# Optimization experiments

Measured on AMD Instinct MI355X. Metric: run time of the kernel, lower is better.

The kernel has to match this reference:

```python
import jax, jax.numpy as jnp
import numpy as np

N, IN_DIM, OUT_DIM = 8192, 512, 256
ALPHA = 0.2
NEG_INF = -9e15


def setup_inputs() -> dict:
    key = jax.random.key(0)
    k1, k2, k3, k4 = jax.random.split(key, 4)
    node_features = jax.random.normal(k1, (N, IN_DIM), dtype=jnp.float32)
    adj_matrix = jax.random.randint(k2, (N, N), 0, 2, dtype=jnp.int32)
    # xavier-uniform linear weight [out,in] -> store as [in,out]
    lim_w = float(np.sqrt(6.0 / (IN_DIM + OUT_DIM)))
    W = jax.random.uniform(k3, (IN_DIM, OUT_DIM), dtype=jnp.float32, minval=-lim_w, maxval=lim_w)
    b = jnp.zeros((OUT_DIM,), dtype=jnp.float32)
    # attention Linear(2*out_dim, 1): weight a [2*out_dim], bias scalar
    lim_a = float(np.sqrt(6.0 / (2 * OUT_DIM + 1)))
    a = jax.random.uniform(k4, (2 * OUT_DIM,), dtype=jnp.float32, minval=-lim_a, maxval=lim_a)
    a_bias = jnp.zeros((), dtype=jnp.float32)
    return {"adj_matrix": adj_matrix, "node_features": node_features, "W": W, "b": b, "a": a, "a_bias": a_bias}


def reference(adj_matrix, node_features, W, b, a, a_bias):
    # h = Linear(node_features); dropout is identity in eval mode
    h = node_features @ W + b                     # [N, D]
    # attention(cat(h_i, h_j)) == h_i @ a_l + h_j @ a_r + a_bias
    a_l, a_r = a[:OUT_DIM], a[OUT_DIM:]
    e_l = h @ a_l                                 # [N]
    e_r = h @ a_r                                 # [N]
    e = jax.nn.leaky_relu(e_l[:, None] + e_r[None, :] + a_bias, ALPHA)  # [N, N]
    scores = jnp.where(adj_matrix > 0, e, NEG_INF)
    attention = jax.nn.softmax(scores, axis=1)    # [N, N]
    h_prime = attention @ h                       # [N, D]
    return h_prime
```

## Files before the change

### kernel.cpp

```cpp
#include <hip/hip_runtime.h>

#define N 8192
#define DIN 512
#define DOUT 256
#define ALPHA 0.2f
#define NEG_INF -9.0e15f

typedef __attribute__((ext_vector_type(8))) short bf16x8;
typedef __attribute__((ext_vector_type(4))) float f32x4;
typedef __attribute__((ext_vector_type(4))) int   i32x4;

__device__ __forceinline__ unsigned f2bf_u(float f) {
    unsigned u = __builtin_bit_cast(unsigned, f);
    return (u + 0x7fffu + ((u >> 16) & 1u)) >> 16;
}
__device__ __forceinline__ unsigned pack2bf(float lo, float hi) {
    return f2bf_u(lo) | (f2bf_u(hi) << 16);
}
__device__ __forceinline__ float bf2f(ushort u) {
    return __builtin_bit_cast(float, (unsigned)u << 16);
}
union U4BF8 { uint4 u; bf16x8 v; };

__device__ __forceinline__ void async_copy16(const ushort* g, ushort* l) {
    __builtin_amdgcn_global_load_lds(
        (const __attribute__((address_space(1))) unsigned*)g,
        (__attribute__((address_space(3))) unsigned*)l, 16, 0, 0);
}

__global__ __launch_bounds__(256) void wb_kernel(const float* __restrict__ W,
                                                 ushort* __restrict__ WB) {
    const int g = blockIdx.x * 256 + threadIdx.x;
    const int c = g & 255, k8 = g >> 8;
    const float* wp = W + (size_t)(k8 * 8) * DOUT + c;
    U4BF8 o;
    o.u.x = pack2bf(wp[0 * DOUT], wp[1 * DOUT]);
    o.u.y = pack2bf(wp[2 * DOUT], wp[3 * DOUT]);
    o.u.z = pack2bf(wp[4 * DOUT], wp[5 * DOUT]);
    o.u.w = pack2bf(wp[6 * DOUT], wp[7 * DOUT]);
    *(uint4*)(WB + (size_t)g * 8) = o.u;
}

__global__ __launch_bounds__(256) void h_kernel(
        const float* __restrict__ X, const ushort* __restrict__ WB,
        const float* __restrict__ bvec, const float* __restrict__ a,
        ushort* __restrict__ hB, float* __restrict__ el, float* __restrict__ er)
{
    __shared__ float red[4][64][65];
    __shared__ float elr[2][4][16];
    const int t = threadIdx.x;
    const int w = t >> 6, l = t & 63, q = l >> 4, n = l & 15;
    const int i0 = blockIdx.x * 16;
    f32x4 acc[16];
    #pragma unroll
    for (int ct = 0; ct < 16; ++ct) acc[ct] = (f32x4){0.f, 0.f, 0.f, 0.f};
    const float* xp = X + (size_t)(i0 + n) * DIN + q * 8;

    #pragma unroll
    for (int ks = 0; ks < 4; ++ks) {
        const int k0 = w * 128 + ks * 32;
        const float4 x0 = *(const float4*)(xp + k0);
        const float4 x1 = *(const float4*)(xp + k0 + 4);
        U4BF8 pa;
        pa.u.x = pack2bf(x0.x, x0.y); pa.u.y = pack2bf(x0.z, x0.w);
        pa.u.z = pack2bf(x1.x, x1.y); pa.u.w = pack2bf(x1.z, x1.w);
        const ushort* wbp = WB + ((k0 >> 3) + q) * 2048 + n * 8;
        bf16x8 bfr[16];
        #pragma unroll
        for (int ct = 0; ct < 16; ++ct) bfr[ct] = *(const bf16x8*)(wbp + ct * 128);
        #pragma unroll
        for (int ct = 0; ct < 16; ++ct)
            acc[ct] = __builtin_amdgcn_mfma_f32_16x16x32_bf16(pa.v, bfr[ct], acc[ct], 0, 0, 0);
    }
    #pragma unroll
    for (int ct = 0; ct < 16; ++ct)
        #pragma unroll
        for (int r = 0; r < 4; ++r) red[w][l][ct * 4 + r] = acc[ct][r];
    __syncthreads();

    float pl[4] = {0.f, 0.f, 0.f, 0.f}, pr[4] = {0.f, 0.f, 0.f, 0.f};
    const int hbase = (blockIdx.x * 2 + (q >> 1)) * 2048 + n * 8 + (q & 1) * 4;
    #pragma unroll
    for (int c2 = 0; c2 < 4; ++c2) {
        const int ct = w * 4 + c2;
        const float bb = bvec[ct * 16 + n];
        const float al = a[ct * 16 + n];
        const float ar = a[DOUT + ct * 16 + n];
        float v[4];
        #pragma unroll
        for (int r = 0; r < 4; ++r) {
            v[r] = red[0][l][ct * 4 + r] + red[1][l][ct * 4 + r]
                 + red[2][l][ct * 4 + r] + red[3][l][ct * 4 + r] + bb;
            pl[r] += v[r] * al;
            pr[r] += v[r] * ar;
        }
        ushort4 hp;
        hp.x = (ushort)f2bf_u(v[0]); hp.y = (ushort)f2bf_u(v[1]);
        hp.z = (ushort)f2bf_u(v[2]); hp.w = (ushort)f2bf_u(v[3]);
        *(ushort4*)&hB[hbase + ct * 128] = hp;
    }
    #pragma unroll
    for (int r = 0; r < 4; ++r) {
        #pragma unroll
        for (int off = 1; off < 16; off <<= 1) {
            pl[r] += __shfl_xor(pl[r], off);
            pr[r] += __shfl_xor(pr[r], off);
        }
    }
    if (n == 0) {
        #pragma unroll
        for (int r = 0; r < 4; ++r) {
            elr[0][w][q * 4 + r] = pl[r];
            elr[1][w][q * 4 + r] = pr[r];
        }
    }
    __syncthreads();
    if (t < 16) {
        el[i0 + t] = elr[0][0][t] + elr[0][1][t] + elr[0][2][t] + elr[0][3][t];
        er[i0 + t] = elr[1][0][t] + elr[1][1][t] + elr[1][2][t] + elr[1][3][t];
    }
}

__global__ __launch_bounds__(512, 1) void attn_kernel(
        const int* __restrict__ adj, const float* __restrict__ el,
        const float* __restrict__ er, const float* __restrict__ ab,
        const ushort* __restrict__ hB, ushort* __restrict__ pout,
        float* __restrict__ plsum)
{
    __shared__ ushort stage[2][32768];
    __shared__ float ers[2048];
    const int t = threadIdx.x;
    const int w = t >> 6, l = t & 63, q = l >> 4, n = l & 15;
    const int rb = blockIdx.x >> 2, jq = blockIdx.x & 3;
    const int j0 = jq * 2048;
    const int row = rb * 128 + w * 16 + n;
    const float elm = el[row] + ab[0];
    const int* alp = adj + (size_t)row * N + j0 + q * 8;

    f32x4 acc[16];
    #pragma unroll
    for (int ct = 0; ct < 16; ++ct) acc[ct] = (f32x4){0.f, 0.f, 0.f, 0.f};
    float lsum = 0.f;

    *(float4*)&ers[t * 4] = *(const float4*)&er[j0 + t * 4];
    i32x4 a[8];
    #pragma unroll
    for (int kg = 0; kg < 4; ++kg) {
        a[2 * kg]     = *(const i32x4*)(alp + kg * 32);
        a[2 * kg + 1] = *(const i32x4*)(alp + kg * 32 + 4);
    }
    {
        const ushort* g = hB + (size_t)j0 * 256 + t * 8;
        ushort* lb = &stage[0][t * 8];
        #pragma unroll
        for (int i = 0; i < 8; ++i) async_copy16(g + i * 4096, lb + i * 4096);
    }

    for (int s = 0; s < 16; ++s) {
        __syncthreads();
        i32x4 aa[8];
        #pragma unroll
        for (int i = 0; i < 8; ++i) aa[i] = a[i];
        if (s < 15) {
            const int* ap = alp + (s + 1) * 128;
            #pragma unroll
            for (int kg = 0; kg < 4; ++kg) {
                a[2 * kg]     = *(const i32x4*)(ap + kg * 32);
                a[2 * kg + 1] = *(const i32x4*)(ap + kg * 32 + 4);
            }
            const ushort* g = hB + (size_t)(j0 + (s + 1) * 128) * 256 + t * 8;
            ushort* lb = &stage[(s + 1) & 1][t * 8];
            #pragma unroll
            for (int i = 0; i < 8; ++i) async_copy16(g + i * 4096, lb + i * 4096);
        }
        U4BF8 pa[4];
        #pragma unroll
        for (int kg = 0; kg < 4; ++kg) {
            const float4 e0 = *(const float4*)&ers[s * 128 + kg * 32 + q * 8];
            const float4 e1 = *(const float4*)&ers[s * 128 + kg * 32 + q * 8 + 4];
            const i32x4 a0 = aa[2 * kg], a1 = aa[2 * kg + 1];
            float v, p0, p1, p2, p3, p4, p5, p6, p7;
            v = elm + e0.x; v = fmaxf(v, ALPHA * v); p0 = __expf(a0.x > 0 ? v : NEG_INF);
            v = elm + e0.y; v = fmaxf(v, ALPHA * v); p1 = __expf(a0.y > 0 ? v : NEG_INF);
            v = elm + e0.z; v = fmaxf(v, ALPHA * v); p2 = __expf(a0.z > 0 ? v : NEG_INF);
            v = elm + e0.w; v = fmaxf(v, ALPHA * v); p3 = __expf(a0.w > 0 ? v : NEG_INF);
            v = elm + e1.x; v = fmaxf(v, ALPHA * v); p4 = __expf(a1.x > 0 ? v : NEG_INF);
            v = elm + e1.y; v = fmaxf(v, ALPHA * v); p5 = __expf(a1.y > 0 ? v : NEG_INF);
            v = elm + e1.z; v = fmaxf(v, ALPHA * v); p6 = __expf(a1.z > 0 ? v : NEG_INF);
            v = elm + e1.w; v = fmaxf(v, ALPHA * v); p7 = __expf(a1.w > 0 ? v : NEG_INF);
            lsum += p0 + p1 + p2 + p3 + p4 + p5 + p6 + p7;
            pa[kg].u.x = pack2bf(p0, p1); pa[kg].u.y = pack2bf(p2, p3);
            pa[kg].u.z = pack2bf(p4, p5); pa[kg].u.w = pack2bf(p6, p7);
        }
        #pragma unroll
        for (int kg = 0; kg < 4; ++kg) {
            const ushort* sb = &stage[s & 1][(kg * 4 + q) * 2048 + n * 8];
            #pragma unroll
            for (int ct = 0; ct < 16; ++ct) {
                const bf16x8 bf = *(const bf16x8*)(sb + ct * 128);
                acc[ct] = __builtin_amdgcn_mfma_f32_16x16x32_bf16(pa[kg].v, bf, acc[ct], 0, 0, 0);
            }
        }
    }

    lsum += __shfl_xor(lsum, 16);
    lsum += __shfl_xor(lsum, 32);
    if (l < 16) plsum[(size_t)jq * N + row] = lsum;

    ushort* pb = pout + ((size_t)jq * N + rb * 128 + w * 16 + q * 4) * 256 + n;
    #pragma unroll
    for (int ct = 0; ct < 16; ++ct)
        #pragma unroll
        for (int r = 0; r < 4; ++r)
            __builtin_nontemporal_store((ushort)f2bf_u(acc[ct][r]),
                                        pb + (size_t)r * 256 + ct * 16);
}

__global__ __launch_bounds__(256) void combine_kernel(
        const ushort* __restrict__ pout, const float* __restrict__ plsum,
        float* __restrict__ out)
{
    const int t = threadIdx.x;
    const int row = blockIdx.x * 4 + (t >> 6);
    const int c = (t & 63) * 4;
    const size_t idx = (size_t)row * 256 + c;
    const size_t qs = (size_t)N * 256;
    const ushort4 v0 = *(const ushort4*)&pout[idx];
    const ushort4 v1 = *(const ushort4*)&pout[idx + qs];
    const ushort4 v2 = *(const ushort4*)&pout[idx + 2 * qs];
    const ushort4 v3 = *(const ushort4*)&pout[idx + 3 * qs];
    const float li = 1.0f / (plsum[row] + plsum[N + row]
                           + plsum[2 * N + row] + plsum[3 * N + row]);
    float4 o;
    o.x = (bf2f(v0.x) + bf2f(v1.x) + bf2f(v2.x) + bf2f(v3.x)) * li;
    o.y = (bf2f(v0.y) + bf2f(v1.y) + bf2f(v2.y) + bf2f(v3.y)) * li;
    o.z = (bf2f(v0.z) + bf2f(v1.z) + bf2f(v2.z) + bf2f(v3.z)) * li;
    o.w = (bf2f(v0.w) + bf2f(v1.w) + bf2f(v2.w) + bf2f(v3.w)) * li;
    *(float4*)&out[idx] = o;
}

extern "C" void kernel_launch(void* const* d_in, const int* in_sizes, int n_in,
                              void* d_out, int out_size, void* d_ws, size_t ws_size,
                              hipStream_t stream) {
    const int*   adj = (const int*)  d_in[0];
    const float* X   = (const float*)d_in[1];
    const float* W   = (const float*)d_in[2];
    const float* b   = (const float*)d_in[3];
    const float* a   = (const float*)d_in[4];
    const float* ab  = (const float*)d_in[5];
    float* out = (float*)d_out;

    ushort* hB    = (ushort*)d_ws;
    ushort* WB    = hB + (size_t)N * DOUT;
    float*  el    = (float*)(WB + (size_t)DIN * DOUT);
    float*  er    = el + N;
    float*  plsum = er + N;
    ushort* pout  = (ushort*)(plsum + 4 * N);

    wb_kernel<<<dim3(64), dim3(256), 0, stream>>>(W, WB);
    h_kernel<<<dim3(N / 16), dim3(256), 0, stream>>>(X, WB, b, a, hB, el, er);
    attn_kernel<<<dim3(256), dim3(512), 0, stream>>>(adj, el, er, ab, hB, pout, plsum);
    combine_kernel<<<dim3(N / 4), dim3(256), 0, stream>>>(pout, plsum, out);
}
```

Baseline: 428.0 us.

## Pre-pack adjacency matrix into bitmask before attention kernel

Adds a separate kernel that compresses the int32 adjacency matrix into one bit per entry, in the interleaved order the attention kernel consumes. The attention kernel then loads one 32-bit mask word per step instead of eight 16-byte int vectors, which cuts register pressure and global traffic inside the MFMA loop. In exchange, the full adjacency read moves into an extra kernel launch with byte-granular scattered stores. It also adds a new workspace region for the bits.

```diff
diff --git a/kernel.cpp b/kernel.cpp
--- a/kernel.cpp
+++ b/kernel.cpp
@@ -41,6 +41,24 @@
     *(uint4*)(WB + (size_t)g * 8) = o.u;
 }
 
+__global__ __launch_bounds__(256) void pack_kernel(const int* __restrict__ adj,
+                                                   unsigned char* __restrict__ bits) {
+    const int t = threadIdx.x;
+    const int r = blockIdx.x * 16 + (t >> 4);
+    const int c = t & 15;
+    const int* ap = adj + (size_t)r * N + c * 8;
+    unsigned char* bp = bits + (size_t)r * (N / 8) + (c & 3) * 4 + (c >> 2);
+    for (int s = 0; s < 64; ++s) {
+        const i32x4 a0 = *(const i32x4*)(ap + s * 128);
+        const i32x4 a1 = *(const i32x4*)(ap + s * 128 + 4);
+        unsigned b = (a0.x > 0 ? 1u : 0u)  | (a0.y > 0 ? 2u : 0u)
+                   | (a0.z > 0 ? 4u : 0u)  | (a0.w > 0 ? 8u : 0u)
+                   | (a1.x > 0 ? 16u : 0u) | (a1.y > 0 ? 32u : 0u)
+                   | (a1.z > 0 ? 64u : 0u) | (a1.w > 0 ? 128u : 0u);
+        bp[s * 16] = (unsigned char)b;
+    }
+}
+
 __global__ __launch_bounds__(256) void h_kernel(
         const float* __restrict__ X, const ushort* __restrict__ WB,
         const float* __restrict__ bvec, const float* __restrict__ a,
@@ -122,7 +140,7 @@
 }
 
 __global__ __launch_bounds__(512, 1) void attn_kernel(
-        const int* __restrict__ adj, const float* __restrict__ el,
+        const unsigned char* __restrict__ bits, const float* __restrict__ el,
         const float* __restrict__ er, const float* __restrict__ ab,
         const ushort* __restrict__ hB, ushort* __restrict__ pout,
         float* __restrict__ plsum)
@@ -135,7 +153,7 @@
     const int j0 = jq * 2048;
     const int row = rb * 128 + w * 16 + n;
     const float elm = el[row] + ab[0];
-    const int* alp = adj + (size_t)row * N + j0 + q * 8;
+    const uint* mp = (const uint*)(bits + (size_t)row * (N / 8) + jq * 256) + q;
 
     f32x4 acc[16];
     #pragma unroll
@@ -143,12 +161,7 @@
     float lsum = 0.f;
 
     *(float4*)&ers[t * 4] = *(const float4*)&er[j0 + t * 4];
-    i32x4 a[8];
-    #pragma unroll
-    for (int kg = 0; kg < 4; ++kg) {
-        a[2 * kg]     = *(const i32x4*)(alp + kg * 32);
-        a[2 * kg + 1] = *(const i32x4*)(alp + kg * 32 + 4);
-    }
+    uint mcur = mp[0];
     {
         const ushort* g = hB + (size_t)j0 * 256 + t * 8;
         ushort* lb = &stage[0][t * 8];
@@ -158,16 +171,9 @@
 
     for (int s = 0; s < 16; ++s) {
         __syncthreads();
-        i32x4 aa[8];
-        #pragma unroll
-        for (int i = 0; i < 8; ++i) aa[i] = a[i];
+        const uint mm = mcur;
         if (s < 15) {
-            const int* ap = alp + (s + 1) * 128;
-            #pragma unroll
-            for (int kg = 0; kg < 4; ++kg) {
-                a[2 * kg]     = *(const i32x4*)(ap + kg * 32);
-                a[2 * kg + 1] = *(const i32x4*)(ap + kg * 32 + 4);
-            }
+            mcur = mp[(s + 1) * 4];
             const ushort* g = hB + (size_t)(j0 + (s + 1) * 128) * 256 + t * 8;
             ushort* lb = &stage[(s + 1) & 1][t * 8];
             #pragma unroll
@@ -176,18 +182,18 @@
         U4BF8 pa[4];
         #pragma unroll
         for (int kg = 0; kg < 4; ++kg) {
+            const uint bk = (mm >> (kg * 8)) & 0xffu;
             const float4 e0 = *(const float4*)&ers[s * 128 + kg * 32 + q * 8];
             const float4 e1 = *(const float4*)&ers[s * 128 + kg * 32 + q * 8 + 4];
-            const i32x4 a0 = aa[2 * kg], a1 = aa[2 * kg + 1];
             float v, p0, p1, p2, p3, p4, p5, p6, p7;
-            v = elm + e0.x; v = fmaxf(v, ALPHA * v); p0 = __expf(a0.x > 0 ? v : NEG_INF);
-            v = elm + e0.y; v = fmaxf(v, ALPHA * v); p1 = __expf(a0.y > 0 ? v : NEG_INF);
-            v = elm + e0.z; v = fmaxf(v, ALPHA * v); p2 = __expf(a0.z > 0 ? v : NEG_INF);
-            v = elm + e0.w; v = fmaxf(v, ALPHA * v); p3 = __expf(a0.w > 0 ? v : NEG_INF);
-            v = elm + e1.x; v = fmaxf(v, ALPHA * v); p4 = __expf(a1.x > 0 ? v : NEG_INF);
-            v = elm + e1.y; v = fmaxf(v, ALPHA * v); p5 = __expf(a1.y > 0 ? v : NEG_INF);
-            v = elm + e1.z; v = fmaxf(v, ALPHA * v); p6 = __expf(a1.z > 0 ? v : NEG_INF);
-            v = elm + e1.w; v = fmaxf(v, ALPHA * v); p7 = __expf(a1.w > 0 ? v : NEG_INF);
+            v = elm + e0.x; v = fmaxf(v, ALPHA * v); p0 = __expf(bk & 1u   ? v : NEG_INF);
+            v = elm + e0.y; v = fmaxf(v, ALPHA * v); p1 = __expf(bk & 2u   ? v : NEG_INF);
+            v = elm + e0.z; v = fmaxf(v, ALPHA * v); p2 = __expf(bk & 4u   ? v : NEG_INF);
+            v = elm + e0.w; v = fmaxf(v, ALPHA * v); p3 = __expf(bk & 8u   ? v : NEG_INF);
+            v = elm + e1.x; v = fmaxf(v, ALPHA * v); p4 = __expf(bk & 16u  ? v : NEG_INF);
+            v = elm + e1.y; v = fmaxf(v, ALPHA * v); p5 = __expf(bk & 32u  ? v : NEG_INF);
+            v = elm + e1.z; v = fmaxf(v, ALPHA * v); p6 = __expf(bk & 64u  ? v : NEG_INF);
+            v = elm + e1.w; v = fmaxf(v, ALPHA * v); p7 = __expf(bk & 128u ? v : NEG_INF);
             lsum += p0 + p1 + p2 + p3 + p4 + p5 + p6 + p7;
             pa[kg].u.x = pack2bf(p0, p1); pa[kg].u.y = pack2bf(p2, p3);
             pa[kg].u.z = pack2bf(p4, p5); pa[kg].u.w = pack2bf(p6, p7);
@@ -256,9 +262,11 @@
     float*  er    = el + N;
     float*  plsum = er + N;
     ushort* pout  = (ushort*)(plsum + 4 * N);
+    unsigned char* bits = (unsigned char*)(pout + (size_t)4 * N * DOUT);
 
     wb_kernel<<<dim3(64), dim3(256), 0, stream>>>(W, WB);
+    pack_kernel<<<dim3(N / 16), dim3(256), 0, stream>>>(adj, bits);
     h_kernel<<<dim3(N / 16), dim3(256), 0, stream>>>(X, WB, b, a, hB, el, er);
-    attn_kernel<<<dim3(256), dim3(512), 0, stream>>>(adj, el, er, ab, hB, pout, plsum);
+    attn_kernel<<<dim3(256), dim3(512), 0, stream>>>(bits, el, er, ab, hB, pout, plsum);
     combine_kernel<<<dim3(N / 4), dim3(256), 0, stream>>>(pout, plsum, out);
 }
```

After: 444.2 us. 1.04x slower.

## Process two row tiles per wave over narrower column slices in attention

Applied to the files above, without the earlier changes.

Each wave now computes two 16-row MFMA tiles that share every staged hB tile, so shared-memory operand traffic per MFMA is halved. Each block covers 256 rows and 1024 columns instead of 128 rows and 2048 columns, which doubles the column partials the combine kernel must merge (8 instead of 4). The next adjacency and hB prefetch is now issued after the exponent phase rather than before it. The launch bound asks for 2 blocks per CU, which caps registers while the accumulators double, so spills are a real risk; LDS use also looks too large for two blocks to fit.

```diff
diff --git a/kernel.cpp b/kernel.cpp
--- a/kernel.cpp
+++ b/kernel.cpp
@@ -121,33 +121,40 @@
     }
 }
 
-__global__ __launch_bounds__(512, 1) void attn_kernel(
+__global__ __launch_bounds__(512, 2) void attn_kernel(
         const int* __restrict__ adj, const float* __restrict__ el,
         const float* __restrict__ er, const float* __restrict__ ab,
         const ushort* __restrict__ hB, ushort* __restrict__ pout,
         float* __restrict__ plsum)
 {
     __shared__ ushort stage[2][32768];
-    __shared__ float ers[2048];
+    __shared__ float ers[1024];
     const int t = threadIdx.x;
     const int w = t >> 6, l = t & 63, q = l >> 4, n = l & 15;
-    const int rb = blockIdx.x >> 2, jq = blockIdx.x & 3;
-    const int j0 = jq * 2048;
-    const int row = rb * 128 + w * 16 + n;
-    const float elm = el[row] + ab[0];
-    const int* alp = adj + (size_t)row * N + j0 + q * 8;
-
-    f32x4 acc[16];
-    #pragma unroll
-    for (int ct = 0; ct < 16; ++ct) acc[ct] = (f32x4){0.f, 0.f, 0.f, 0.f};
-    float lsum = 0.f;
-
-    *(float4*)&ers[t * 4] = *(const float4*)&er[j0 + t * 4];
-    i32x4 a[8];
+    const int rb = blockIdx.x >> 3, jq = blockIdx.x & 7;
+    const int j0 = jq * 1024;
+    const int rowA = rb * 256 + w * 32 + n;
+    const float elmA = el[rowA] + ab[0];
+    const float elmB = el[rowA + 16] + ab[0];
+    const int* apA = adj + (size_t)rowA * N + j0 + q * 8;
+    const int* apB = apA + (size_t)16 * N;
+
+    f32x4 acc0[16], acc1[16];
+    #pragma unroll
+    for (int ct = 0; ct < 16; ++ct) {
+        acc0[ct] = (f32x4){0.f, 0.f, 0.f, 0.f};
+        acc1[ct] = (f32x4){0.f, 0.f, 0.f, 0.f};
+    }
+    float lsumA = 0.f, lsumB = 0.f;
+
+    *(float2*)&ers[t * 2] = *(const float2*)&er[j0 + t * 2];
+    i32x4 a[16];
     #pragma unroll
     for (int kg = 0; kg < 4; ++kg) {
-        a[2 * kg]     = *(const i32x4*)(alp + kg * 32);
-        a[2 * kg + 1] = *(const i32x4*)(alp + kg * 32 + 4);
+        a[2 * kg]     = *(const i32x4*)(apA + kg * 32);
+        a[2 * kg + 1] = *(const i32x4*)(apA + kg * 32 + 4);
+        a[8 + 2 * kg] = *(const i32x4*)(apB + kg * 32);
+        a[9 + 2 * kg] = *(const i32x4*)(apB + kg * 32 + 4);
     }
     {
         const ushort* g = hB + (size_t)j0 * 256 + t * 8;
@@ -156,41 +163,52 @@
         for (int i = 0; i < 8; ++i) async_copy16(g + i * 4096, lb + i * 4096);
     }
 
-    for (int s = 0; s < 16; ++s) {
+    for (int s = 0; s < 8; ++s) {
         __syncthreads();
-        i32x4 aa[8];
-        #pragma unroll
-        for (int i = 0; i < 8; ++i) aa[i] = a[i];
-        if (s < 15) {
-            const int* ap = alp + (s + 1) * 128;
+        U4BF8 paA[4], paB[4];
+        #pragma unroll
+        for (int kg = 0; kg < 4; ++kg) {
+            const float4 e0 = *(const float4*)&ers[s * 128 + kg * 32 + q * 8];
+            const float4 e1 = *(const float4*)&ers[s * 128 + kg * 32 + q * 8 + 4];
+            float v, p0, p1, p2, p3, p4, p5, p6, p7;
+            i32x4 a0 = a[2 * kg], a1 = a[2 * kg + 1];
+            v = elmA + e0.x; v = fmaxf(v, ALPHA * v); p0 = __expf(a0.x > 0 ? v : NEG_INF);
+            v = elmA + e0.y; v = fmaxf(v, ALPHA * v); p1 = __expf(a0.y > 0 ? v : NEG_INF);
+            v = elmA + e0.z; v = fmaxf(v, ALPHA * v); p2 = __expf(a0.z > 0 ? v : NEG_INF);
+            v = elmA + e0.w; v = fmaxf(v, ALPHA * v); p3 = __expf(a0.w > 0 ? v : NEG_INF);
+            v = elmA + e1.x; v = fmaxf(v, ALPHA * v); p4 = __expf(a1.x > 0 ? v : NEG_INF);
+            v = elmA + e1.y; v = fmaxf(v, ALPHA * v); p5 = __expf(a1.y > 0 ? v : NEG_INF);
+            v = elmA + e1.z; v = fmaxf(v, ALPHA * v); p6 = __expf(a1.z > 0 ? v : NEG_INF);
+            v = elmA + e1.w; v = fmaxf(v, ALPHA * v); p7 = __expf(a1.w > 0 ? v : NEG_INF);
+            lsumA += p0 + p1 + p2 + p3 + p4 + p5 + p6 + p7;
+            paA[kg].u.x = pack2bf(p0, p1); paA[kg].u.y = pack2bf(p2, p3);
+            paA[kg].u.z = pack2bf(p4, p5); paA[kg].u.w = pack2bf(p6, p7);
+            a0 = a[8 + 2 * kg]; a1 = a[9 + 2 * kg];
+            v = elmB + e0.x; v = fmaxf(v, ALPHA * v); p0 = __expf(a0.x > 0 ? v : NEG_INF);
+            v = elmB + e0.y; v = fmaxf(v, ALPHA * v); p1 = __expf(a0.y > 0 ? v : NEG_INF);
+            v = elmB + e0.z; v = fmaxf(v, ALPHA * v); p2 = __expf(a0.z > 0 ? v : NEG_INF);
+            v = elmB + e0.w; v = fmaxf(v, ALPHA * v); p3 = __expf(a0.w > 0 ? v : NEG_INF);
+            v = elmB + e1.x; v = fmaxf(v, ALPHA * v); p4 = __expf(a1.x > 0 ? v : NEG_INF);
+            v = elmB + e1.y; v = fmaxf(v, ALPHA * v); p5 = __expf(a1.y > 0 ? v : NEG_INF);
+            v = elmB + e1.z; v = fmaxf(v, ALPHA * v); p6 = __expf(a1.z > 0 ? v : NEG_INF);
+            v = elmB + e1.w; v = fmaxf(v, ALPHA * v); p7 = __expf(a1.w > 0 ? v : NEG_INF);
+            lsumB += p0 + p1 + p2 + p3 + p4 + p5 + p6 + p7;
+            paB[kg].u.x = pack2bf(p0, p1); paB[kg].u.y = pack2bf(p2, p3);
+            paB[kg].u.z = pack2bf(p4, p5); paB[kg].u.w = pack2bf(p6, p7);
+        }
+        if (s < 7) {
+            const int off = (s + 1) * 128;
             #pragma unroll
             for (int kg = 0; kg < 4; ++kg) {
-                a[2 * kg]     = *(const i32x4*)(ap + kg * 32);
-                a[2 * kg + 1] = *(const i32x4*)(ap + kg * 32 + 4);
+                a[2 * kg]     = *(const i32x4*)(apA + off + kg * 32);
+                a[2 * kg + 1] = *(const i32x4*)(apA + off + kg * 32 + 4);
+                a[8 + 2 * kg] = *(const i32x4*)(apB + off + kg * 32);
+                a[9 + 2 * kg] = *(const i32x4*)(apB + off + kg * 32 + 4);
             }
-            const ushort* g = hB + (size_t)(j0 + (s + 1) * 128) * 256 + t * 8;
+            const ushort* g = hB + (size_t)(j0 + off) * 256 + t * 8;
             ushort* lb = &stage[(s + 1) & 1][t * 8];
             #pragma unroll
             for (int i = 0; i < 8; ++i) async_copy16(g + i * 4096, lb + i * 4096);
-        }
-        U4BF8 pa[4];
-        #pragma unroll
-        for (int kg = 0; kg < 4; ++kg) {
-            const float4 e0 = *(const float4*)&ers[s * 128 + kg * 32 + q * 8];
-            const float4 e1 = *(const float4*)&ers[s * 128 + kg * 32 + q * 8 + 4];
-            const i32x4 a0 = aa[2 * kg], a1 = aa[2 * kg + 1];
-            float v, p0, p1, p2, p3, p4, p5, p6, p7;
-            v = elm + e0.x; v = fmaxf(v, ALPHA * v); p0 = __expf(a0.x > 0 ? v : NEG_INF);
-            v = elm + e0.y; v = fmaxf(v, ALPHA * v); p1 = __expf(a0.y > 0 ? v : NEG_INF);
-            v = elm + e0.z; v = fmaxf(v, ALPHA * v); p2 = __expf(a0.z > 0 ? v : NEG_INF);
-            v = elm + e0.w; v = fmaxf(v, ALPHA * v); p3 = __expf(a0.w > 0 ? v : NEG_INF);
-            v = elm + e1.x; v = fmaxf(v, ALPHA * v); p4 = __expf(a1.x > 0 ? v : NEG_INF);
-            v = elm + e1.y; v = fmaxf(v, ALPHA * v); p5 = __expf(a1.y > 0 ? v : NEG_INF);
-            v = elm + e1.z; v = fmaxf(v, ALPHA * v); p6 = __expf(a1.z > 0 ? v : NEG_INF);
-            v = elm + e1.w; v = fmaxf(v, ALPHA * v); p7 = __expf(a1.w > 0 ? v : NEG_INF);
-            lsum += p0 + p1 + p2 + p3 + p4 + p5 + p6 + p7;
-            pa[kg].u.x = pack2bf(p0, p1); pa[kg].u.y = pack2bf(p2, p3);
-            pa[kg].u.z = pack2bf(p4, p5); pa[kg].u.w = pack2bf(p6, p7);
         }
         #pragma unroll
         for (int kg = 0; kg < 4; ++kg) {
@@ -198,22 +216,32 @@
             #pragma unroll
             for (int ct = 0; ct < 16; ++ct) {
                 const bf16x8 bf = *(const bf16x8*)(sb + ct * 128);
-                acc[ct] = __builtin_amdgcn_mfma_f32_16x16x32_bf16(pa[kg].v, bf, acc[ct], 0, 0, 0);
+                acc0[ct] = __builtin_amdgcn_mfma_f32_16x16x32_bf16(paA[kg].v, bf, acc0[ct], 0, 0, 0);
+                acc1[ct] = __builtin_amdgcn_mfma_f32_16x16x32_bf16(paB[kg].v, bf, acc1[ct], 0, 0, 0);
             }
         }
     }
 
-    lsum += __shfl_xor(lsum, 16);
-    lsum += __shfl_xor(lsum, 32);
-    if (l < 16) plsum[(size_t)jq * N + row] = lsum;
-
-    ushort* pb = pout + ((size_t)jq * N + rb * 128 + w * 16 + q * 4) * 256 + n;
+    lsumA += __shfl_xor(lsumA, 16);
+    lsumA += __shfl_xor(lsumA, 32);
+    lsumB += __shfl_xor(lsumB, 16);
+    lsumB += __shfl_xor(lsumB, 32);
+    if (l < 16) {
+        plsum[(size_t)jq * N + rowA] = lsumA;
+        plsum[(size_t)jq * N + rowA + 16] = lsumB;
+    }
+
+    ushort* pb0 = pout + ((size_t)jq * N + rb * 256 + w * 32 + q * 4) * 256 + n;
+    ushort* pb1 = pb0 + 16 * 256;
     #pragma unroll
     for (int ct = 0; ct < 16; ++ct)
         #pragma unroll
-        for (int r = 0; r < 4; ++r)
-            __builtin_nontemporal_store((ushort)f2bf_u(acc[ct][r]),
-                                        pb + (size_t)r * 256 + ct * 16);
+        for (int r = 0; r < 4; ++r) {
+            __builtin_nontemporal_store((ushort)f2bf_u(acc0[ct][r]),
+                                        pb0 + (size_t)r * 256 + ct * 16);
+            __builtin_nontemporal_store((ushort)f2bf_u(acc1[ct][r]),
+                                        pb1 + (size_t)r * 256 + ct * 16);
+        }
 }
 
 __global__ __launch_bounds__(256) void combine_kernel(
@@ -225,17 +253,16 @@
     const int c = (t & 63) * 4;
     const size_t idx = (size_t)row * 256 + c;
     const size_t qs = (size_t)N * 256;
-    const ushort4 v0 = *(const ushort4*)&pout[idx];
-    const ushort4 v1 = *(const ushort4*)&pout[idx + qs];
-    const ushort4 v2 = *(const ushort4*)&pout[idx + 2 * qs];
-    const ushort4 v3 = *(const ushort4*)&pout[idx + 3 * qs];
-    const float li = 1.0f / (plsum[row] + plsum[N + row]
-                           + plsum[2 * N + row] + plsum[3 * N + row]);
-    float4 o;
-    o.x = (bf2f(v0.x) + bf2f(v1.x) + bf2f(v2.x) + bf2f(v3.x)) * li;
-    o.y = (bf2f(v0.y) + bf2f(v1.y) + bf2f(v2.y) + bf2f(v3.y)) * li;
-    o.z = (bf2f(v0.z) + bf2f(v1.z) + bf2f(v2.z) + bf2f(v3.z)) * li;
-    o.w = (bf2f(v0.w) + bf2f(v1.w) + bf2f(v2.w) + bf2f(v3.w)) * li;
+    float4 o = {0.f, 0.f, 0.f, 0.f};
+    float ls = 0.f;
+    #pragma unroll
+    for (int p = 0; p < 8; ++p) {
+        const ushort4 v = *(const ushort4*)&pout[idx + p * qs];
+        o.x += bf2f(v.x); o.y += bf2f(v.y); o.z += bf2f(v.z); o.w += bf2f(v.w);
+        ls += plsum[p * N + row];
+    }
+    const float li = 1.0f / ls;
+    o.x *= li; o.y *= li; o.z *= li; o.w *= li;
     *(float4*)&out[idx] = o;
 }
 
@@ -255,7 +282,7 @@
     float*  el    = (float*)(WB + (size_t)DIN * DOUT);
     float*  er    = el + N;
     float*  plsum = er + N;
-    ushort* pout  = (ushort*)(plsum + 4 * N);
+    ushort* pout  = (ushort*)(plsum + 8 * N);
 
     wb_kernel<<<dim3(64), dim3(256), 0, stream>>>(W, WB);
     h_kernel<<<dim3(N / 16), dim3(256), 0, stream>>>(X, WB, b, a, hB, el, er);
```

After: 510.9 us. 1.19x slower.
